# Performance work log

Hardware: AMD Instinct MI355X
Metric: run time of the kernel (lower is better)

Reference implementation:

```python
import jax, jax.numpy as jnp
import numpy as np

NEG_INF = jnp.finfo(jnp.float32).min


def setup_inputs() -> dict:
    key = jax.random.key(0)
    ks = jax.random.split(key, 5)
    B, S, D = 2, 2048, 1024
    std = 0.02
    return {
        "x": jax.random.normal(ks[0], (B, S, D), dtype=jnp.float32),
        "attention_mask": jnp.ones((B, S), dtype=jnp.int32),
        "Wq": jax.random.normal(ks[1], (D, D), dtype=jnp.float32) * std,
        "Wk": jax.random.normal(ks[2], (D, D), dtype=jnp.float32) * std,
        "Wv": jax.random.normal(ks[3], (D, D), dtype=jnp.float32) * std,
        "Wo": jax.random.normal(ks[4], (D, D), dtype=jnp.float32) * std,
    }


def reference(x, attention_mask, Wq, Wk, Wv, Wo):
    B, S, D = x.shape
    H = 16
    Hd = D // H
    scale = jnp.float32(np.sqrt(Hd))

    # F.linear uses W @ x^T, i.e. x @ W.T
    def proj(x, W):
        return jnp.einsum('bsd,ed->bse', x, W).reshape(B, S, H, Hd).transpose(0, 2, 1, 3)

    q = proj(x, Wq)  # [B,H,S,Hd]
    k = proj(x, Wk)
    v = proj(x, Wv)

    scores = jnp.einsum('bhqd,bhkd->bhqk', q, k) / scale  # [B,H,S,S]
    causal = jnp.triu(jnp.ones((S, S), dtype=bool), k=1)
    scores = jnp.where(causal[None, None, :, :], NEG_INF, scores)
    key_pad = (attention_mask == 0)[:, None, None, :]  # [B,1,1,S]
    scores = jnp.where(key_pad, NEG_INF, scores)

    attn = jax.nn.softmax(scores, axis=-1)
    out = jnp.einsum('bhqk,bhkd->bhqd', attn, v)  # [B,H,S,Hd]
    out = out.transpose(0, 2, 1, 3).reshape(B, S, D)
    return jnp.einsum('bsd,ed->bse', out, Wo)
```

## Files before the change

kernel.cpp:

```cpp
#include <hip/hip_runtime.h>
#include <hip/hip_bf16.h>

typedef __attribute__((ext_vector_type(8))) short bf16x8;
typedef __attribute__((ext_vector_type(4))) short bf16x4;
typedef __attribute__((ext_vector_type(4))) float f32x4;

#define LOG2E 1.4426950408889634f
#define MBIAS 11.541560327111707f
#define NEGF  -3.0e38f

__device__ __forceinline__ void gl_lds16(const void* g, void* l) {
  __builtin_amdgcn_global_load_lds((const __attribute__((address_space(1))) void*)g,
                                   (__attribute__((address_space(3))) void*)l, 16, 0, 0);
}

__device__ __forceinline__ ushort f2bu(float x) {
  __hip_bfloat16 h = __float2bfloat16(x);
  return *(ushort*)&h;
}

__device__ __forceinline__ unsigned int fbits(float x) {
  union { float f; unsigned int u; } c; c.f = x; return c.u;
}

__global__ __launch_bounds__(256)
void cast_all_k(const float* __restrict__ x, const float* __restrict__ a, const float* __restrict__ b,
                const float* __restrict__ c, const float* __restrict__ d,
                ushort* __restrict__ ox, ushort* __restrict__ oa, ushort* __restrict__ ob,
                ushort* __restrict__ oc, ushort* __restrict__ od) {
  int i = blockIdx.x * 256 + threadIdx.x;
  const float* src; ushort* dst; int j;
  if (i < 1048576) {
    src = x; dst = ox; j = i;
  } else {
    int k = i - 1048576;
    int wsel = k >> 18; j = k & 262143;
    src = wsel == 0 ? a : wsel == 1 ? b : wsel == 2 ? c : d;
    dst = wsel == 0 ? oa : wsel == 1 ? ob : wsel == 2 ? oc : od;
  }
  float4 f = ((const float4*)src)[j];
  ushort4 u;
  u.x = f2bu(f.x); u.y = f2bu(f.y); u.z = f2bu(f.z); u.w = f2bu(f.w);
  ((ushort4*)dst)[j] = u;
}

template<int OUT_BF16>
__device__ __forceinline__ void gemm_body(const ushort* __restrict__ A, const ushort* __restrict__ B,
                                          void* __restrict__ C, int M, int N, int Kd, float scale,
                                          int bm, int bn, ushort (*As)[4096], ushort (*Bs)[4096]) {
  const int t  = threadIdx.x;
  const int l  = t & 63;
  const int w  = t >> 6;
  const int lr = l & 15, lg = l >> 4;
  const int wr = (w >> 1) * 64, wc = (w & 1) * 64;

  auto stage = [&](int buf, int ktE) {
    int idx = t, row = idx >> 2, ch = idx & 3;
    gl_lds16(A + (size_t)(bm + row) * Kd + ktE + ch * 8, &As[buf][idx * 8]);
    gl_lds16(B + (size_t)(bn + row) * Kd + ktE + ch * 8, &Bs[buf][idx * 8]);
    idx = t + 256; row = idx >> 2; ch = idx & 3;
    gl_lds16(A + (size_t)(bm + row) * Kd + ktE + ch * 8, &As[buf][idx * 8]);
    gl_lds16(B + (size_t)(bn + row) * Kd + ktE + ch * 8, &Bs[buf][idx * 8]);
  };

  f32x4 acc[4][4] = {};
  const int nK = Kd >> 5;

  stage(0, 0);
  stage(1, 32);
  int cur = 0;
  for (int k5 = 0; k5 < nK; ++k5) {
    if (k5 + 2 < nK) {
      int nb = cur + 2; if (nb >= 3) nb -= 3;
      stage(nb, (k5 + 2) << 5);
      asm volatile("s_waitcnt vmcnt(8)" ::: "memory");
    } else if (k5 + 1 < nK) {
      asm volatile("s_waitcnt vmcnt(4)" ::: "memory");
    } else {
      asm volatile("s_waitcnt vmcnt(0)" ::: "memory");
    }
    __builtin_amdgcn_s_barrier();

    bf16x8 af[4], bfr[4];
#pragma unroll
    for (int m = 0; m < 4; ++m)
      af[m] = *(const bf16x8*)&As[cur][(wr + m * 16 + lr) * 32 + lg * 8];
#pragma unroll
    for (int n = 0; n < 4; ++n)
      bfr[n] = *(const bf16x8*)&Bs[cur][(wc + n * 16 + lr) * 32 + lg * 8];
#pragma unroll
    for (int m = 0; m < 4; ++m)
#pragma unroll
      for (int n = 0; n < 4; ++n)
        acc[m][n] = __builtin_amdgcn_mfma_f32_16x16x32_bf16(af[m], bfr[n], acc[m][n], 0, 0, 0);

    __builtin_amdgcn_s_barrier();
    ++cur; if (cur >= 3) cur -= 3;
  }

#pragma unroll
  for (int m = 0; m < 4; ++m)
#pragma unroll
    for (int n = 0; n < 4; ++n)
#pragma unroll
      for (int j = 0; j < 4; ++j) {
        int row = bm + wr + m * 16 + lg * 4 + j;
        int col = bn + wc + n * 16 + lr;
        float v = acc[m][n][j] * scale;
        if (OUT_BF16) {
          ((ushort*)C)[(size_t)row * N + col] = f2bu(v);
        } else {
          ((float*)C)[(size_t)row * N + col] = v;
        }
      }
}

__global__ __launch_bounds__(256)
void gemm_qkv(const ushort* __restrict__ A, const ushort* __restrict__ Wq, const ushort* __restrict__ Wk,
              const ushort* __restrict__ Wv, ushort* __restrict__ Qo, ushort* __restrict__ Ko,
              ushort* __restrict__ Vo, int M, int Kd) {
  __shared__ __attribute__((aligned(16))) ushort As[3][4096];
  __shared__ __attribute__((aligned(16))) ushort Bs[3][4096];
  int by = blockIdx.y;
  int which = by >> 3;
  const ushort* B = which == 0 ? Wq : which == 1 ? Wk : Wv;
  ushort* C       = which == 0 ? Qo : which == 1 ? Ko : Vo;
  float scale = which == 0 ? 0.125f : 1.0f;
  gemm_body<1>(A, B, C, M, 1024, Kd, scale, blockIdx.x * 128, (by & 7) * 128, As, Bs);
}

__global__ __launch_bounds__(256)
void gemm_out64(const ushort* __restrict__ A, const ushort* __restrict__ B, float* __restrict__ C,
                int M, int N, int Kd) {
  __shared__ __attribute__((aligned(16))) ushort As[3][2048];
  __shared__ __attribute__((aligned(16))) ushort Bs[3][4096];
  const int t  = threadIdx.x;
  const int l  = t & 63;
  const int w  = t >> 6;
  const int lr = l & 15, lg = l >> 4;
  const int wr = (w >> 1) * 32, wc = (w & 1) * 64;
  const int bm = blockIdx.x * 64, bn = blockIdx.y * 128;

  auto stage = [&](int buf, int ktE) {
    int idx = t, row = idx >> 2, ch = idx & 3;
    gl_lds16(A + (size_t)(bm + row) * Kd + ktE + ch * 8, &As[buf][idx * 8]);
    row = idx >> 2; ch = idx & 3;
    gl_lds16(B + (size_t)(bn + row) * Kd + ktE + ch * 8, &Bs[buf][idx * 8]);
    idx = t + 256; row = idx >> 2; ch = idx & 3;
    gl_lds16(B + (size_t)(bn + row) * Kd + ktE + ch * 8, &Bs[buf][idx * 8]);
  };

  f32x4 acc[2][4] = {};
  const int nK = Kd >> 5;

  stage(0, 0);
  stage(1, 32);
  int cur = 0;
  for (int k5 = 0; k5 < nK; ++k5) {
    if (k5 + 2 < nK) {
      int nb = cur + 2; if (nb >= 3) nb -= 3;
      stage(nb, (k5 + 2) << 5);
      asm volatile("s_waitcnt vmcnt(6)" ::: "memory");
    } else if (k5 + 1 < nK) {
      asm volatile("s_waitcnt vmcnt(3)" ::: "memory");
    } else {
      asm volatile("s_waitcnt vmcnt(0)" ::: "memory");
    }
    __builtin_amdgcn_s_barrier();

    bf16x8 af[2], bfr[4];
#pragma unroll
    for (int m = 0; m < 2; ++m)
      af[m] = *(const bf16x8*)&As[cur][(wr + m * 16 + lr) * 32 + lg * 8];
#pragma unroll
    for (int n = 0; n < 4; ++n)
      bfr[n] = *(const bf16x8*)&Bs[cur][(wc + n * 16 + lr) * 32 + lg * 8];
#pragma unroll
    for (int m = 0; m < 2; ++m)
#pragma unroll
      for (int n = 0; n < 4; ++n)
        acc[m][n] = __builtin_amdgcn_mfma_f32_16x16x32_bf16(af[m], bfr[n], acc[m][n], 0, 0, 0);

    __builtin_amdgcn_s_barrier();
    ++cur; if (cur >= 3) cur -= 3;
  }

#pragma unroll
  for (int m = 0; m < 2; ++m)
#pragma unroll
    for (int n = 0; n < 4; ++n)
#pragma unroll
      for (int j = 0; j < 4; ++j) {
        int row = bm + wr + m * 16 + lg * 4 + j;
        int col = bn + wc + n * 16 + lr;
        C[(size_t)row * N + col] = acc[m][n][j];
      }
}

__device__ __forceinline__ void fixed_sm(f32x4 s4[4], bf16x8& pa0_out, bf16x8& pa1_out) {
#pragma unroll
  for (int c = 0; c < 4; ++c)
#pragma unroll
    for (int j = 0; j < 4; ++j)
      s4[c][j] = exp2f(fmaf(s4[c][j], LOG2E, -MBIAS));
  union { bf16x8 v; unsigned int w[4]; } pa0, pa1;
#pragma unroll
  for (int c = 0; c < 2; ++c) {
    pa0.w[2 * c + 0] = __builtin_amdgcn_perm(fbits(s4[c][1]), fbits(s4[c][0]), 0x07060302u);
    pa0.w[2 * c + 1] = __builtin_amdgcn_perm(fbits(s4[c][3]), fbits(s4[c][2]), 0x07060302u);
    pa1.w[2 * c + 0] = __builtin_amdgcn_perm(fbits(s4[c + 2][1]), fbits(s4[c + 2][0]), 0x07060302u);
    pa1.w[2 * c + 1] = __builtin_amdgcn_perm(fbits(s4[c + 2][3]), fbits(s4[c + 2][2]), 0x07060302u);
  }
  pa0_out = pa0.v;
  pa1_out = pa1.v;
}

__global__ __launch_bounds__(512, 4)
void attn_k(const ushort* __restrict__ Q, const ushort* __restrict__ K,
            const ushort* __restrict__ V, const int* __restrict__ mask,
            ushort* __restrict__ O) {
  const int S = 2048, D = 1024;
  __shared__ __attribute__((aligned(16))) ushort Ks[4][4096];
  __shared__ __attribute__((aligned(16))) ushort Vs[4][4096];
  __shared__ unsigned long long Msb[32];

  const int t = threadIdx.x;
  const int l = t & 63, w = t >> 6;
  const int lr = l & 15, lg = l >> 4;

  int f = blockIdx.x;
  int pp = (f >> 3) & 15;
  int ss = ((f >> 8) & 1) ? 15 - pp : pp;
  int bh = (f & 7) | (((f >> 7) & 3) << 3);
  int h = bh & 15, b = bh >> 4;
  const int nt = 2 * ss + 2;
  const int np = ss + 1;
  const int q0 = ss * 128;
  const bool hiW = (w >> 2);
  const int npO = hiW ? np : np - 1;
  const int cdi = w & 3;
  const size_t bS = (size_t)b * S;

  const ushort* qptr = Q + (bS + q0 + w * 16 + lr) * D + h * 64;
  bf16x8 qf0 = *(const bf16x8*)(qptr + lg * 8);
  bf16x8 qf1 = *(const bf16x8*)(qptr + 32 + lg * 8);

  const ushort* Kbh = K + bS * D + h * 64;
  const ushort* Vbh = V + bS * D + h * 64;
  const int* mbase = mask + bS;

  bf16x8 onesf;
#pragma unroll
  for (int i = 0; i < 8; ++i) onesf[i] = (short)0x3F80;

  int koffA[4], koffB[4];
#pragma unroll
  for (int c = 0; c < 4; ++c) {
    int row = c * 16 + lr;
    koffA[c] = row * 64 + ((lg ^ (row & 7)) << 3);
    koffB[c] = row * 64 + (((4 + lg) ^ (row & 7)) << 3);
  }
  int voff[4];
#pragma unroll
  for (int dt = 0; dt < 4; ++dt) voff[dt] = dt * 1024 + lg * 64 + lr * 4;

  for (int kk = w; kk < nt; kk += 8) {
    unsigned long long mb = __ballot(mbase[kk * 64 + l] != 0);
    if (l == 0) Msb[kk] = mb;
  }
  asm volatile("s_waitcnt lgkmcnt(0)" ::: "memory");
  __builtin_amdgcn_sched_barrier(0);

  f32x4 lsum = {0.f, 0.f, 0.f, 0.f};
  f32x4 oE[4] = {}, oO[4] = {};

  auto stage = [&](int p) {
    int s0 = (p & 1) << 1;
    int k0 = 2 * p, k1 = 2 * p + 1;
    { int idx = t; int row = idx >> 3, ch = idx & 7;
      size_t go = (size_t)row * D + ((ch ^ (row & 7)) * 8);
      gl_lds16(Kbh + (size_t)(k0 * 64) * D + go, &Ks[s0][idx * 8]);
      gl_lds16(Kbh + (size_t)(k1 * 64) * D + go, &Ks[s0 + 1][idx * 8]); }
    { int idx = t; int dg = idx >> 7, kq = (idx >> 3) & 15, jj = (idx >> 1) & 3, hf = idx & 1;
      size_t go = (size_t)(kq * 4 + jj) * D + dg * 16 + hf * 8;
      gl_lds16(Vbh + (size_t)(k0 * 64) * D + go, &Vs[s0][idx * 8]);
      gl_lds16(Vbh + (size_t)(k1 * 64) * D + go, &Vs[s0 + 1][idx * 8]); }
  };

  stage(0);
  if (np > 1) stage(1);

  for (int p = 0; p < np; ++p) {
    const int s0 = (p & 1) << 1;
    if (p + 1 < np) asm volatile("s_waitcnt vmcnt(4)" ::: "memory");
    else            asm volatile("s_waitcnt vmcnt(0)" ::: "memory");
    __builtin_amdgcn_s_barrier();

    const bool actO  = (p < npO);
    const bool diagE = (!hiW) && (p == ss);
    const bool diagO = hiW && (p == ss);
    const int cmaxE = diagE ? cdi : 3;
    const int cmaxO = diagO ? cdi : 3;
    unsigned long long mbE = Msb[2 * p];
    unsigned long long mbO = Msb[2 * p + 1];

    f32x4 sE[4], sO[4];
#pragma unroll
    for (int c = 0; c < 4; ++c) {
      if (c <= cmaxE) {
        bf16x8 kf0 = *(const bf16x8*)&Ks[s0][koffA[c]];
        bf16x8 kf1 = *(const bf16x8*)&Ks[s0][koffB[c]];
        f32x4 sc = {0.f, 0.f, 0.f, 0.f};
        sc = __builtin_amdgcn_mfma_f32_16x16x32_bf16(kf0, qf0, sc, 0, 0, 0);
        sc = __builtin_amdgcn_mfma_f32_16x16x32_bf16(kf1, qf1, sc, 0, 0, 0);
        if (diagE && c == cmaxE) {
          int qg = cdi * 16 + lr, kb = c * 16 + lg * 4;
#pragma unroll
          for (int j = 0; j < 4; ++j)
            if (kb + j > qg) sc[j] = NEGF;
        }
        sE[c] = sc;
      } else {
        sE[c] = (f32x4){NEGF, NEGF, NEGF, NEGF};
      }
      if (actO) {
        if (c <= cmaxO) {
          bf16x8 kf0 = *(const bf16x8*)&Ks[s0 + 1][koffA[c]];
          bf16x8 kf1 = *(const bf16x8*)&Ks[s0 + 1][koffB[c]];
          f32x4 sc = {0.f, 0.f, 0.f, 0.f};
          sc = __builtin_amdgcn_mfma_f32_16x16x32_bf16(kf0, qf0, sc, 0, 0, 0);
          sc = __builtin_amdgcn_mfma_f32_16x16x32_bf16(kf1, qf1, sc, 0, 0, 0);
          if (diagO && c == cmaxO) {
            int qg = cdi * 16 + lr, kb = c * 16 + lg * 4;
#pragma unroll
            for (int j = 0; j < 4; ++j)
              if (kb + j > qg) sc[j] = NEGF;
          }
          sO[c] = sc;
        } else {
          sO[c] = (f32x4){NEGF, NEGF, NEGF, NEGF};
        }
      }
    }

    if (~mbE != 0ull) {
#pragma unroll
      for (int c = 0; c < 4; ++c)
#pragma unroll
        for (int j = 0; j < 4; ++j)
          if (!((mbE >> (c * 16 + lg * 4 + j)) & 1)) sE[c][j] = NEGF;
    }
    if (actO && (~mbO != 0ull)) {
#pragma unroll
      for (int c = 0; c < 4; ++c)
#pragma unroll
        for (int j = 0; j < 4; ++j)
          if (!((mbO >> (c * 16 + lg * 4 + j)) & 1)) sO[c][j] = NEGF;
    }

    bf16x8 paE0, paE1;
    fixed_sm(sE, paE0, paE1);
    lsum = __builtin_amdgcn_mfma_f32_16x16x32_bf16(paE0, onesf, lsum, 0, 0, 0);
    lsum = __builtin_amdgcn_mfma_f32_16x16x32_bf16(paE1, onesf, lsum, 0, 0, 0);
#pragma unroll
    for (int dt = 0; dt < 4; ++dt) {
      const __attribute__((address_space(3))) ushort* vp =
          (const __attribute__((address_space(3))) ushort*)&Vs[s0][0] + voff[dt];
      bf16x4 h0, h1, h2, h3;
      asm volatile(
          "ds_read_b64_tr_b16 %0, %4\n\t"
          "ds_read_b64_tr_b16 %1, %4 offset:512\n\t"
          "ds_read_b64_tr_b16 %2, %4 offset:1024\n\t"
          "ds_read_b64_tr_b16 %3, %4 offset:1536\n\t"
          "s_waitcnt lgkmcnt(0)"
          : "=&v"(h0), "=&v"(h1), "=&v"(h2), "=&v"(h3)
          : "v"(vp));
      bf16x8 vb0 = __builtin_shufflevector(h0, h1, 0, 1, 2, 3, 4, 5, 6, 7);
      bf16x8 vb1 = __builtin_shufflevector(h2, h3, 0, 1, 2, 3, 4, 5, 6, 7);
      oE[dt] = __builtin_amdgcn_mfma_f32_16x16x32_bf16(paE0, vb0, oE[dt], 0, 0, 0);
      oE[dt] = __builtin_amdgcn_mfma_f32_16x16x32_bf16(paE1, vb1, oE[dt], 0, 0, 0);
    }

    if (actO) {
      bf16x8 paO0, paO1;
      fixed_sm(sO, paO0, paO1);
      lsum = __builtin_amdgcn_mfma_f32_16x16x32_bf16(paO0, onesf, lsum, 0, 0, 0);
      lsum = __builtin_amdgcn_mfma_f32_16x16x32_bf16(paO1, onesf, lsum, 0, 0, 0);
#pragma unroll
      for (int dt = 0; dt < 4; ++dt) {
        const __attribute__((address_space(3))) ushort* vp =
            (const __attribute__((address_space(3))) ushort*)&Vs[s0 + 1][0] + voff[dt];
        bf16x4 h0, h1, h2, h3;
        asm volatile(
            "ds_read_b64_tr_b16 %0, %4\n\t"
            "ds_read_b64_tr_b16 %1, %4 offset:512\n\t"
            "ds_read_b64_tr_b16 %2, %4 offset:1024\n\t"
            "ds_read_b64_tr_b16 %3, %4 offset:1536\n\t"
            "s_waitcnt lgkmcnt(0)"
            : "=&v"(h0), "=&v"(h1), "=&v"(h2), "=&v"(h3)
            : "v"(vp));
        bf16x8 vb0 = __builtin_shufflevector(h0, h1, 0, 1, 2, 3, 4, 5, 6, 7);
        bf16x8 vb1 = __builtin_shufflevector(h2, h3, 0, 1, 2, 3, 4, 5, 6, 7);
        oO[dt] = __builtin_amdgcn_mfma_f32_16x16x32_bf16(paO0, vb0, oO[dt], 0, 0, 0);
        oO[dt] = __builtin_amdgcn_mfma_f32_16x16x32_bf16(paO1, vb1, oO[dt], 0, 0, 0);
      }
    }

    __builtin_amdgcn_s_barrier();
    if (p + 2 < np) stage(p + 2);
  }

  float iv0 = 1.0f / lsum[0];
  float iv1 = 1.0f / lsum[1];
  float iv2 = 1.0f / lsum[2];
  float iv3 = 1.0f / lsum[3];
#pragma unroll
  for (int dt = 0; dt < 4; ++dt) {
    size_t col = (size_t)h * 64 + dt * 16 + lr;
    size_t r0 = bS + q0 + w * 16 + lg * 4;
    O[(r0 + 0) * D + col] = f2bu((oE[dt][0] + oO[dt][0]) * iv0);
    O[(r0 + 1) * D + col] = f2bu((oE[dt][1] + oO[dt][1]) * iv1);
    O[(r0 + 2) * D + col] = f2bu((oE[dt][2] + oO[dt][2]) * iv2);
    O[(r0 + 3) * D + col] = f2bu((oE[dt][3] + oO[dt][3]) * iv3);
  }
}

extern "C" void kernel_launch(void* const* d_in, const int* in_sizes, int n_in,
                              void* d_out, int out_size, void* d_ws, size_t ws_size,
                              hipStream_t stream) {
  const float* x    = (const float*)d_in[0];
  const int*   mask = (const int*)d_in[1];
  const float* Wq   = (const float*)d_in[2];
  const float* Wk   = (const float*)d_in[3];
  const float* Wv   = (const float*)d_in[4];
  const float* Wo   = (const float*)d_in[5];
  float* out = (float*)d_out;

  const int B = 2, S = 2048, D = 1024;
  const int M = B * S;

  char* ws = (char*)d_ws;
  ushort* xb  = (ushort*)(ws);
  ushort* wqb = (ushort*)(ws + (8ull  << 20));
  ushort* wkb = (ushort*)(ws + (10ull << 20));
  ushort* wvb = (ushort*)(ws + (12ull << 20));
  ushort* wob = (ushort*)(ws + (14ull << 20));
  ushort* Qb  = (ushort*)(ws + (16ull << 20));
  ushort* Kb  = (ushort*)(ws + (24ull << 20));
  ushort* Vb  = (ushort*)(ws + (32ull << 20));
  ushort* AO  = (ushort*)(ws + (40ull << 20));

  cast_all_k<<<8192, 256, 0, stream>>>(x, Wq, Wk, Wv, Wo, xb, wqb, wkb, wvb, wob);

  dim3 gq(M / 128, 24);
  gemm_qkv<<<gq, 256, 0, stream>>>(xb, wqb, wkb, wvb, Qb, Kb, Vb, M, D);

  attn_k<<<512, 512, 0, stream>>>(Qb, Kb, Vb, mask, AO);

  dim3 go(M / 64, D / 128);
  gemm_out64<<<go, 256, 0, stream>>>(AO, wob, out, M, D, D);
}
```

Baseline: 112.1 us.

## Swizzle GEMM LDS layout and remap blocks to XCDs for L2 locality

Applies an XOR swizzle on the 16-byte chunk index in both GEMM kernels, on the global-to-LDS staging side and on the fragment reads, to cut LDS bank conflicts when waves read bf16x8 fragments. Both GEMMs now use a flat 1D grid with manual block-index remapping so that blocks landing on the same XCD (round-robin by blockIdx mod 8) share neighbouring A row tiles, which should improve L2 reuse. The unused M parameter is dropped. The change depends on the round-robin dispatch assumption, and the attention kernel is untouched, so the benefit is limited to the GEMM portion.

```diff
diff --git a/kernel.cpp b/kernel.cpp
--- a/kernel.cpp
+++ b/kernel.cpp
@@ -46,7 +46,7 @@
 
 template<int OUT_BF16>
 __device__ __forceinline__ void gemm_body(const ushort* __restrict__ A, const ushort* __restrict__ B,
-                                          void* __restrict__ C, int M, int N, int Kd, float scale,
+                                          void* __restrict__ C, int N, int Kd, float scale,
                                           int bm, int bn, ushort (*As)[4096], ushort (*Bs)[4096]) {
   const int t  = threadIdx.x;
   const int l  = t & 63;
@@ -56,11 +56,11 @@
 
   auto stage = [&](int buf, int ktE) {
     int idx = t, row = idx >> 2, ch = idx & 3;
-    gl_lds16(A + (size_t)(bm + row) * Kd + ktE + ch * 8, &As[buf][idx * 8]);
-    gl_lds16(B + (size_t)(bn + row) * Kd + ktE + ch * 8, &Bs[buf][idx * 8]);
+    gl_lds16(A + (size_t)(bm + row) * Kd + ktE + ((ch ^ (row & 3)) * 8), &As[buf][idx * 8]);
+    gl_lds16(B + (size_t)(bn + row) * Kd + ktE + ((ch ^ (row & 3)) * 8), &Bs[buf][idx * 8]);
     idx = t + 256; row = idx >> 2; ch = idx & 3;
-    gl_lds16(A + (size_t)(bm + row) * Kd + ktE + ch * 8, &As[buf][idx * 8]);
-    gl_lds16(B + (size_t)(bn + row) * Kd + ktE + ch * 8, &Bs[buf][idx * 8]);
+    gl_lds16(A + (size_t)(bm + row) * Kd + ktE + ((ch ^ (row & 3)) * 8), &As[buf][idx * 8]);
+    gl_lds16(B + (size_t)(bn + row) * Kd + ktE + ((ch ^ (row & 3)) * 8), &Bs[buf][idx * 8]);
   };
 
   f32x4 acc[4][4] = {};
@@ -83,11 +83,15 @@
 
     bf16x8 af[4], bfr[4];
 #pragma unroll
-    for (int m = 0; m < 4; ++m)
-      af[m] = *(const bf16x8*)&As[cur][(wr + m * 16 + lr) * 32 + lg * 8];
-#pragma unroll
-    for (int n = 0; n < 4; ++n)
-      bfr[n] = *(const bf16x8*)&Bs[cur][(wc + n * 16 + lr) * 32 + lg * 8];
+    for (int m = 0; m < 4; ++m) {
+      int row = wr + m * 16 + lr;
+      af[m] = *(const bf16x8*)&As[cur][row * 32 + ((lg ^ (row & 3)) << 3)];
+    }
+#pragma unroll
+    for (int n = 0; n < 4; ++n) {
+      int row = wc + n * 16 + lr;
+      bfr[n] = *(const bf16x8*)&Bs[cur][row * 32 + ((lg ^ (row & 3)) << 3)];
+    }
 #pragma unroll
     for (int m = 0; m < 4; ++m)
 #pragma unroll
@@ -118,20 +122,23 @@
 __global__ __launch_bounds__(256)
 void gemm_qkv(const ushort* __restrict__ A, const ushort* __restrict__ Wq, const ushort* __restrict__ Wk,
               const ushort* __restrict__ Wv, ushort* __restrict__ Qo, ushort* __restrict__ Ko,
-              ushort* __restrict__ Vo, int M, int Kd) {
+              ushort* __restrict__ Vo, int Kd) {
   __shared__ __attribute__((aligned(16))) ushort As[3][4096];
   __shared__ __attribute__((aligned(16))) ushort Bs[3][4096];
-  int by = blockIdx.y;
+  int f = blockIdx.x;
+  int xcd = f & 7, i = f >> 3;
+  int bx = xcd * 4 + (i & 3);
+  int by = i >> 2;
   int which = by >> 3;
   const ushort* B = which == 0 ? Wq : which == 1 ? Wk : Wv;
   ushort* C       = which == 0 ? Qo : which == 1 ? Ko : Vo;
   float scale = which == 0 ? 0.125f : 1.0f;
-  gemm_body<1>(A, B, C, M, 1024, Kd, scale, blockIdx.x * 128, (by & 7) * 128, As, Bs);
+  gemm_body<1>(A, B, C, 1024, Kd, scale, bx * 128, (by & 7) * 128, As, Bs);
 }
 
 __global__ __launch_bounds__(256)
 void gemm_out64(const ushort* __restrict__ A, const ushort* __restrict__ B, float* __restrict__ C,
-                int M, int N, int Kd) {
+                int N, int Kd) {
   __shared__ __attribute__((aligned(16))) ushort As[3][2048];
   __shared__ __attribute__((aligned(16))) ushort Bs[3][4096];
   const int t  = threadIdx.x;
@@ -139,15 +146,17 @@
   const int w  = t >> 6;
   const int lr = l & 15, lg = l >> 4;
   const int wr = (w >> 1) * 32, wc = (w & 1) * 64;
-  const int bm = blockIdx.x * 64, bn = blockIdx.y * 128;
+  int f = blockIdx.x;
+  int xcd = f & 7, i = f >> 3;
+  const int bm = (xcd * 8 + (i & 7)) * 64;
+  const int bn = (i >> 3) * 128;
 
   auto stage = [&](int buf, int ktE) {
     int idx = t, row = idx >> 2, ch = idx & 3;
-    gl_lds16(A + (size_t)(bm + row) * Kd + ktE + ch * 8, &As[buf][idx * 8]);
-    row = idx >> 2; ch = idx & 3;
-    gl_lds16(B + (size_t)(bn + row) * Kd + ktE + ch * 8, &Bs[buf][idx * 8]);
+    gl_lds16(A + (size_t)(bm + row) * Kd + ktE + ((ch ^ (row & 3)) * 8), &As[buf][idx * 8]);
+    gl_lds16(B + (size_t)(bn + row) * Kd + ktE + ((ch ^ (row & 3)) * 8), &Bs[buf][idx * 8]);
     idx = t + 256; row = idx >> 2; ch = idx & 3;
-    gl_lds16(B + (size_t)(bn + row) * Kd + ktE + ch * 8, &Bs[buf][idx * 8]);
+    gl_lds16(B + (size_t)(bn + row) * Kd + ktE + ((ch ^ (row & 3)) * 8), &Bs[buf][idx * 8]);
   };
 
   f32x4 acc[2][4] = {};
@@ -170,11 +179,15 @@
 
     bf16x8 af[2], bfr[4];
 #pragma unroll
-    for (int m = 0; m < 2; ++m)
-      af[m] = *(const bf16x8*)&As[cur][(wr + m * 16 + lr) * 32 + lg * 8];
-#pragma unroll
-    for (int n = 0; n < 4; ++n)
-      bfr[n] = *(const bf16x8*)&Bs[cur][(wc + n * 16 + lr) * 32 + lg * 8];
+    for (int m = 0; m < 2; ++m) {
+      int row = wr + m * 16 + lr;
+      af[m] = *(const bf16x8*)&As[cur][row * 32 + ((lg ^ (row & 3)) << 3)];
+    }
+#pragma unroll
+    for (int n = 0; n < 4; ++n) {
+      int row = wc + n * 16 + lr;
+      bfr[n] = *(const bf16x8*)&Bs[cur][row * 32 + ((lg ^ (row & 3)) << 3)];
+    }
 #pragma unroll
     for (int m = 0; m < 2; ++m)
 #pragma unroll
@@ -452,11 +465,9 @@
 
   cast_all_k<<<8192, 256, 0, stream>>>(x, Wq, Wk, Wv, Wo, xb, wqb, wkb, wvb, wob);
 
-  dim3 gq(M / 128, 24);
-  gemm_qkv<<<gq, 256, 0, stream>>>(xb, wqb, wkb, wvb, Qb, Kb, Vb, M, D);
+  gemm_qkv<<<768, 256, 0, stream>>>(xb, wqb, wkb, wvb, Qb, Kb, Vb, D);
 
   attn_k<<<512, 512, 0, stream>>>(Qb, Kb, Vb, mask, AO);
 
-  dim3 go(M / 64, D / 128);
-  gemm_out64<<<go, 256, 0, stream>>>(AO, wob, out, M, D, D);
-}
+  gemm_out64<<<512, 256, 0, stream>>>(AO, wob, out, D, D);
+}
```

After: 112.2 us (median of 2 runs). About the same (+0.1%).
